# Kernel optimization log

Measured on AMD Instinct MI355X. Metric: run time of the kernel, lower is better.

Reference implementation:

```python
import jax, jax.numpy as jnp
import numpy as np

T_THRESH = 1.0  # t_thresh init arg
W_I = 1.0       # call() passes w_i=1
W_LEAK_MAX = 0.2  # RandomUniform(0, w_leak_start) initializer range


@jax.custom_vjp
def spike(v):
    # theta_one with 'flat' surrogate: heaviside forward, pass-through (flat) gradient
    return (v > 0).astype(v.dtype)

def _spike_fwd(v):
    return spike(v), None

def _spike_bwd(_, g):
    return (g,)

spike.defvjp(_spike_fwd, _spike_bwd)


def setup_inputs() -> dict:
    key = jax.random.key(0)
    k1, k2 = jax.random.split(key)
    B, T, C = 128, 1000, 512
    x = jax.random.normal(k1, (B, T, C), dtype=jnp.float32)
    w_leak = jax.random.uniform(k2, (C,), dtype=jnp.float32, minval=0.0, maxval=W_LEAK_MAX)
    return {"x": x, "w_leak": w_leak}


def reference(x, w_leak):
    # x: [B, T, C]; w_leak: [C]
    xt = jnp.swapaxes(x, 0, 1)  # [T, B, C] for scan over time

    def step(Vm, x_t):
        # theta_forget(t_thresh - Vm): hard reset gate (1 if Vm < thresh else 0)
        keep = (T_THRESH - Vm > 0).astype(Vm.dtype)
        Vm = jax.nn.relu(W_I * x_t + (1.0 - w_leak) * Vm * keep)
        return Vm, spike(Vm - T_THRESH)

    Vm0 = jnp.zeros_like(xt[0])  # [B, C]
    _, spikes = jax.lax.scan(step, Vm0, xt)  # spikes: [T, B, C]
    return jnp.swapaxes(spikes, 0, 1)  # [B, T, C]
```

## Files before the change

kernel.cpp:

```cpp
#include <hip/hip_runtime.h>


constexpr int Bn  = 128;
constexpr int Tn  = 1000;
constexpr int Cn  = 512;
constexpr int C4  = Cn / 4;
constexpr int U   = 20;
constexpr int NCH = Tn / U;

#define LIF_STEP(vm, oml, xin, sp)            \
    {                                          \
        float p_ = (oml) * (vm);               \
        p_ = ((vm) < 1.0f) ? p_ : 0.0f;        \
        float t_ = (xin) + p_;                 \
        (vm) = fmaxf(t_, 0.0f);                \
        (sp) = ((vm) > 1.0f) ? 1.0f : 0.0f;    \
    }

__global__ __launch_bounds__(64) void lif_kernel(const float4* __restrict__ x4,
                                                 const float*  __restrict__ w_leak,
                                                 float4* __restrict__ out4) {
    const int bid = blockIdx.x;
    const int b   = bid >> 1;
    const int c4  = ((bid & 1) << 6) | threadIdx.x;

    const float4 wl  = reinterpret_cast<const float4*>(w_leak)[c4];
    const float omlx = 1.0f - wl.x;
    const float omly = 1.0f - wl.y;
    const float omlz = 1.0f - wl.z;
    const float omlw = 1.0f - wl.w;

    const size_t base = (size_t)b * Tn * C4 + c4;
    const float4* xp = x4 + base;
    float4*       op = out4 + base;

    float vmx = 0.0f, vmy = 0.0f, vmz = 0.0f, vmw = 0.0f;
    float4 bufA[U], bufB[U];

#pragma unroll
    for (int i = 0; i < U; ++i) bufA[i] = xp[i * C4];
    __builtin_amdgcn_sched_barrier(0);

    for (int ch = 0; ch < NCH; ch += 2) {
        {
            const float4* xn = xp + (size_t)(ch + 1) * U * C4;
#pragma unroll
            for (int i = 0; i < U; ++i) bufB[i] = xn[i * C4];
        }
        __builtin_amdgcn_sched_barrier(0);
        {
            float4* on = op + (size_t)ch * U * C4;
#pragma unroll
            for (int i = 0; i < U; ++i) {
                float4 xv = bufA[i];
                float4 s;
                LIF_STEP(vmx, omlx, xv.x, s.x);
                LIF_STEP(vmy, omly, xv.y, s.y);
                LIF_STEP(vmz, omlz, xv.z, s.z);
                LIF_STEP(vmw, omlw, xv.w, s.w);
                on[i * C4] = s;
            }
        }
        __builtin_amdgcn_sched_barrier(0);
        if (ch + 2 < NCH) {
            const float4* xn = xp + (size_t)(ch + 2) * U * C4;
#pragma unroll
            for (int i = 0; i < U; ++i) bufA[i] = xn[i * C4];
        }
        __builtin_amdgcn_sched_barrier(0);
        {
            float4* on = op + (size_t)(ch + 1) * U * C4;
#pragma unroll
            for (int i = 0; i < U; ++i) {
                float4 xv = bufB[i];
                float4 s;
                LIF_STEP(vmx, omlx, xv.x, s.x);
                LIF_STEP(vmy, omly, xv.y, s.y);
                LIF_STEP(vmz, omlz, xv.z, s.z);
                LIF_STEP(vmw, omlw, xv.w, s.w);
                on[i * C4] = s;
            }
        }
        __builtin_amdgcn_sched_barrier(0);
    }
}

extern "C" void kernel_launch(void* const* d_in, const int* in_sizes, int n_in,
                              void* d_out, int out_size, void* d_ws, size_t ws_size,
                              hipStream_t stream) {
    const float4* x      = (const float4*)d_in[0];
    const float*  w_leak = (const float*)d_in[1];
    float4*       out    = (float4*)d_out;

    lif_kernel<<<256, 64, 0, stream>>>(x, w_leak, out);
}
```

Baseline: 435.3 us.

## Use float2 per thread with 512 blocks and a rolling single-buffer prefetch

Each thread now handles two channels instead of four, doubling the grid to 512 wavefronts so more CUs participate in this latency-bound sequential scan. The double buffer with sched barriers becomes a single rolling buffer, where each element's next-chunk load is issued just after it is consumed, plus a peeled final chunk. Narrower float2 accesses mean more memory instructions per byte, and dropping the sched barriers leaves load scheduling to the compiler.

```diff
diff --git a/kernel.cpp b/kernel.cpp
--- a/kernel.cpp
+++ b/kernel.cpp
@@ -4,7 +4,7 @@
 constexpr int Bn  = 128;
 constexpr int Tn  = 1000;
 constexpr int Cn  = 512;
-constexpr int C4  = Cn / 4;
+constexpr int C2  = Cn / 2;
 constexpr int U   = 20;
 constexpr int NCH = Tn / U;
 
@@ -17,80 +17,60 @@
         (sp) = ((vm) > 1.0f) ? 1.0f : 0.0f;    \
     }
 
-__global__ __launch_bounds__(64) void lif_kernel(const float4* __restrict__ x4,
+__global__ __launch_bounds__(64) void lif_kernel(const float2* __restrict__ x2,
                                                  const float*  __restrict__ w_leak,
-                                                 float4* __restrict__ out4) {
-    const int bid = blockIdx.x;
-    const int b   = bid >> 1;
-    const int c4  = ((bid & 1) << 6) | threadIdx.x;
+                                                 float2* __restrict__ out2) {
+    const int gid = blockIdx.x * 64 + threadIdx.x;
+    const int c2  = gid & (C2 - 1);
+    const int b   = gid >> 8;
 
-    const float4 wl  = reinterpret_cast<const float4*>(w_leak)[c4];
+    const float2 wl  = reinterpret_cast<const float2*>(w_leak)[c2];
     const float omlx = 1.0f - wl.x;
     const float omly = 1.0f - wl.y;
-    const float omlz = 1.0f - wl.z;
-    const float omlw = 1.0f - wl.w;
 
-    const size_t base = (size_t)b * Tn * C4 + c4;
-    const float4* xp = x4 + base;
-    float4*       op = out4 + base;
+    const size_t base = (size_t)b * Tn * C2 + c2;
+    const float2* xp = x2 + base;
+    float2*       op = out2 + base;
 
-    float vmx = 0.0f, vmy = 0.0f, vmz = 0.0f, vmw = 0.0f;
-    float4 bufA[U], bufB[U];
+    float vmx = 0.0f, vmy = 0.0f;
+    float2 buf[U];
 
 #pragma unroll
-    for (int i = 0; i < U; ++i) bufA[i] = xp[i * C4];
-    __builtin_amdgcn_sched_barrier(0);
+    for (int i = 0; i < U; ++i) buf[i] = xp[i * C2];
 
-    for (int ch = 0; ch < NCH; ch += 2) {
-        {
-            const float4* xn = xp + (size_t)(ch + 1) * U * C4;
+    for (int ch = 0; ch < NCH - 1; ++ch) {
+        const float2* xn = xp + (size_t)(ch + 1) * U * C2;
+        float2*       on = op + (size_t)ch * U * C2;
 #pragma unroll
-            for (int i = 0; i < U; ++i) bufB[i] = xn[i * C4];
+        for (int i = 0; i < U; ++i) {
+            float2 xv = buf[i];
+            buf[i] = xn[i * C2];
+            float2 s;
+            LIF_STEP(vmx, omlx, xv.x, s.x);
+            LIF_STEP(vmy, omly, xv.y, s.y);
+            on[i * C2] = s;
         }
-        __builtin_amdgcn_sched_barrier(0);
-        {
-            float4* on = op + (size_t)ch * U * C4;
+    }
+
+    {
+        float2* on = op + (size_t)(NCH - 1) * U * C2;
 #pragma unroll
-            for (int i = 0; i < U; ++i) {
-                float4 xv = bufA[i];
-                float4 s;
-                LIF_STEP(vmx, omlx, xv.x, s.x);
-                LIF_STEP(vmy, omly, xv.y, s.y);
-                LIF_STEP(vmz, omlz, xv.z, s.z);
-                LIF_STEP(vmw, omlw, xv.w, s.w);
-                on[i * C4] = s;
-            }
+        for (int i = 0; i < U; ++i) {
+            float2 xv = buf[i];
+            float2 s;
+            LIF_STEP(vmx, omlx, xv.x, s.x);
+            LIF_STEP(vmy, omly, xv.y, s.y);
+            on[i * C2] = s;
         }
-        __builtin_amdgcn_sched_barrier(0);
-        if (ch + 2 < NCH) {
-            const float4* xn = xp + (size_t)(ch + 2) * U * C4;
-#pragma unroll
-            for (int i = 0; i < U; ++i) bufA[i] = xn[i * C4];
-        }
-        __builtin_amdgcn_sched_barrier(0);
-        {
-            float4* on = op + (size_t)(ch + 1) * U * C4;
-#pragma unroll
-            for (int i = 0; i < U; ++i) {
-                float4 xv = bufB[i];
-                float4 s;
-                LIF_STEP(vmx, omlx, xv.x, s.x);
-                LIF_STEP(vmy, omly, xv.y, s.y);
-                LIF_STEP(vmz, omlz, xv.z, s.z);
-                LIF_STEP(vmw, omlw, xv.w, s.w);
-                on[i * C4] = s;
-            }
-        }
-        __builtin_amdgcn_sched_barrier(0);
     }
 }
 
 extern "C" void kernel_launch(void* const* d_in, const int* in_sizes, int n_in,
                               void* d_out, int out_size, void* d_ws, size_t ws_size,
                               hipStream_t stream) {
-    const float4* x      = (const float4*)d_in[0];
+    const float2* x      = (const float2*)d_in[0];
     const float*  w_leak = (const float*)d_in[1];
-    float4*       out    = (float4*)d_out;
+    float2*       out    = (float2*)d_out;
 
-    lif_kernel<<<256, 64, 0, stream>>>(x, w_leak, out);
+    lif_kernel<<<512, 64, 0, stream>>>(x, w_leak, out);
 }
```

After: 436.5 us. No clear change (+0.3%).
